# Performance work log

Measured on AMD Instinct MI355X. Metric: run time of the kernel, lower is better.

The kernel has to match this reference:

```python
import jax, jax.numpy as jnp
import numpy as np

B, N, E, H = 8, 512, 1024, 128   # graphs, nodes, edges, hidden
T = 8                             # num_edge_types
HOPS = 3                          # graph_hops


def setup_inputs() -> dict:
    key = jax.random.key(0)
    ks = jax.random.split(key, 10)
    node_feature = jax.random.normal(ks[0], (B, N, H), dtype=jnp.float32)
    edge_vec = jax.random.randint(ks[1], (B, E), 0, T)  # per-edge type ids
    # sparse incidence matrices (one-hot edge endpoints), as the scipy .A densification does
    src = jax.random.randint(ks[2], (B, E), 0, N)
    tgt = jax.random.randint(ks[3], (B, E), 0, N)
    node2edge = jax.nn.one_hot(src, N, dtype=jnp.float32)                 # [B,E,N]
    edge2node = jnp.swapaxes(jax.nn.one_hot(tgt, N, dtype=jnp.float32), 1, 2)  # [B,N,E]
    s = 0.02  # xavier-ish init scale
    edge_weight_tensor = jax.random.normal(ks[4], (T, H * H), dtype=jnp.float32) * s
    Wz = jax.random.normal(ks[5], (2 * H, H), dtype=jnp.float32) * s
    Wr = jax.random.normal(ks[6], (2 * H, H), dtype=jnp.float32) * s
    Wt = jax.random.normal(ks[7], (2 * H, H), dtype=jnp.float32) * s
    Wf = jax.random.normal(ks[8], (4 * H, H), dtype=jnp.float32) * s
    bf = jnp.zeros((H,), dtype=jnp.float32)
    return {"node_feature": node_feature, "edge_vec": edge_vec,
            "node2edge": node2edge, "edge2node": edge2node,
            "edge_weight_tensor": edge_weight_tensor,
            "Wz": Wz, "Wr": Wr, "Wt": Wt, "Wf": Wf, "bf": bf}


def reference(node_feature, edge_vec, node2edge, edge2node,
              edge_weight_tensor, Wz, Wr, Wt, Wf, bf):
    Hd = node_feature.shape[-1]
    # gather per-edge weight matrices once (edge_vec is constant across hops)
    Wedge = edge_weight_tensor[edge_vec].reshape(edge_vec.shape + (Hd, Hd))  # [B,E,H,H]

    def mp(h, n2e, e2n):
        emb = jnp.einsum('ben,bnh->beh', n2e, h)          # gather node states to edges
        new = jnp.einsum('behd,bed->beh', Wedge, emb)     # per-edge-type matvec
        return jnp.einsum('bne,beh->bnh', e2n, new)       # scatter-aggregate to nodes

    def gru_step(h, a):
        x = jnp.concatenate([h, a], axis=-1)
        z = jax.nn.sigmoid(x @ Wz)
        r = jax.nn.sigmoid(x @ Wr)
        t = jnp.tanh(jnp.concatenate([r * h, a], axis=-1) @ Wt)
        return (1.0 - z) * h + z * t

    h = node_feature
    for _ in range(HOPS):
        bw = mp(h, node2edge, edge2node)
        fw = mp(h, jnp.swapaxes(edge2node, 1, 2), jnp.swapaxes(node2edge, 1, 2))
        # GatedFusion(fw, bw)
        z = jax.nn.sigmoid(jnp.concatenate([fw, bw, fw * bw, fw - bw], axis=-1) @ Wf + bf)
        agg = (1.0 - z) * fw + z * bw
        h = gru_step(h, agg)
    return h
```

## Files before the change

kernel.cpp:

```cpp
#include <hip/hip_runtime.h>

#define Bb 8
#define Nn 512
#define Ee 1024
#define Hh 128
#define Tt 8
#define FPAD 132

__device__ __forceinline__ float sigm(float x){ return 1.0f/(1.0f + __expf(-x)); }
__device__ __forceinline__ float tanh_fast(float x){ return 2.0f/(1.0f + __expf(-2.0f*x)) - 1.0f; }

__device__ __forceinline__ void fma4(float* acc, float4 x, float4 w0, float4 w1, float4 w2, float4 w3){
  acc[0] += x.x*w0.x + x.y*w1.x + x.z*w2.x + x.w*w3.x;
  acc[1] += x.x*w0.y + x.y*w1.y + x.z*w2.y + x.w*w3.y;
  acc[2] += x.x*w0.z + x.y*w1.z + x.z*w2.z + x.w*w3.z;
  acc[3] += x.x*w0.w + x.y*w1.w + x.z*w2.w + x.w*w3.w;
}

__global__ void k_extract(const float4* __restrict__ n2e, const float4* __restrict__ e2n,
                          int* __restrict__ src, int* __restrict__ tgt){
  const int total1 = Bb*Ee*Nn/4;
  for (int i = blockIdx.x*blockDim.x + threadIdx.x; i < total1; i += gridDim.x*blockDim.x){
    float4 v = n2e[i];
    if (v.x!=0.f || v.y!=0.f || v.z!=0.f || v.w!=0.f){
      int base = i*4;
      int row = base >> 9;
      int n   = base & 511;
      if (v.x!=0.f) src[row] = n;
      if (v.y!=0.f) src[row] = n+1;
      if (v.z!=0.f) src[row] = n+2;
      if (v.w!=0.f) src[row] = n+3;
    }
  }
  const int total2 = Bb*Nn*Ee/4;
  for (int i = blockIdx.x*blockDim.x + threadIdx.x; i < total2; i += gridDim.x*blockDim.x){
    float4 v = e2n[i];
    if (v.x!=0.f || v.y!=0.f || v.z!=0.f || v.w!=0.f){
      int base = i*4;
      int row = base >> 10;
      int e   = base & 1023;
      int b = row >> 9, n = row & 511;
      int* tp = tgt + b*Ee;
      if (v.x!=0.f) tp[e]   = n;
      if (v.y!=0.f) tp[e+1] = n;
      if (v.z!=0.f) tp[e+2] = n;
      if (v.w!=0.f) tp[e+3] = n;
    }
  }
}

__global__ void k_transW(const float* __restrict__ W, float* __restrict__ WT){
  int i = blockIdx.x*blockDim.x + threadIdx.x;
  if (i >= Tt*Hh*Hh) return;
  int t = i >> 14;
  int h = (i >> 7) & 127;
  int d = i & 127;
  WT[(t*Hh + d)*Hh + h] = W[i];
}

__global__ void k_prep(const float* __restrict__ Wf, float* __restrict__ Ff){
  int i = blockIdx.x*blockDim.x + threadIdx.x;
  if (i >= 384*Hh) return;
  int r = i >> 7, c = i & 127;
  float v;
  if (r < 128)      v = Wf[r*Hh + c] + Wf[(r+384)*Hh + c];
  else if (r < 256) v = Wf[r*Hh + c] - Wf[(r+256)*Hh + c];
  else              v = Wf[r*Hh + c];
  Ff[i] = v;
}

__global__ void k_sort(const int* __restrict__ ev, int* __restrict__ order, int* __restrict__ offs){
  __shared__ int cnt[Tt], offs_s[Tt+1], pos[Tt];
  int b = blockIdx.x, tid = threadIdx.x;
  if (tid < Tt) cnt[tid] = 0;
  __syncthreads();
  for (int e = tid; e < Ee; e += blockDim.x) atomicAdd(&cnt[ev[b*Ee+e]], 1);
  __syncthreads();
  if (tid == 0){ offs_s[0]=0; for (int t=0;t<Tt;t++) offs_s[t+1]=offs_s[t]+cnt[t]; }
  __syncthreads();
  if (tid < Tt) pos[tid] = offs_s[tid];
  if (tid < Tt+1) offs[b*(Tt+1)+tid] = offs_s[tid];
  __syncthreads();
  for (int e = tid; e < Ee; e += blockDim.x){
    int t = ev[b*Ee+e];
    int p = atomicAdd(&pos[t], 1);
    order[b*Ee + p] = e;
  }
}

__global__ __launch_bounds__(256) void k_edge_mp(
    const float* __restrict__ h, const float* __restrict__ WT,
    const int* __restrict__ order, const int* __restrict__ offs,
    const int* __restrict__ src, const int* __restrict__ tgt,
    float* __restrict__ bw, float* __restrict__ fw)
{
  int x = blockIdx.x;
  int dir = x & 1, bt = x >> 1, t = bt & 7, b = bt >> 3;
  int beg = offs[b*(Tt+1)+t], end = offs[b*(Tt+1)+t+1];
  int chunk0 = beg + blockIdx.y*32;
  if (chunk0 >= end) return;
  const int* gI = dir ? tgt : src;
  const int* sI = dir ? src : tgt;
  float* out = dir ? fw : bw;

  __shared__ float sEmb[32][FPAD];
  __shared__ int sNode[32];
  int tid = threadIdx.x, lane = tid & 63, w = tid >> 6;
  int e0 = (lane >> 3)*4;
  int c0 = w*32 + (lane & 7)*4;
  const float* __restrict__ Wg = WT + t*Hh*Hh + c0;

  for (int chunk = chunk0; chunk < end; chunk += gridDim.y*32){
    int ne = min(32, end - chunk);
    __syncthreads();
    {
      int ir = tid >> 5, k0 = (tid & 31)*4;
      #pragma unroll
      for (int rr = 0; rr < 4; ++rr){
        int e = ir + rr*8;
        float4 v = {0.f,0.f,0.f,0.f};
        if (e < ne){
          int eid = order[b*Ee + chunk + e];
          v = *(const float4*)&h[(size_t)(b*Nn + gI[b*Ee + eid])*Hh + k0];
        }
        *(float4*)&sEmb[e][k0] = v;
      }
      if (tid < 32){
        int nd = -1;
        if (tid < ne){ int eid = order[b*Ee + chunk + tid]; nd = sI[b*Ee + eid]; }
        sNode[tid] = nd;
      }
    }
    __syncthreads();

    float acc[4][4] = {};
    #pragma unroll 4
    for (int k = 0; k < Hh; k += 4){
      float4 w0 = *(const float4*)&Wg[(size_t)(k+0)*Hh];
      float4 w1 = *(const float4*)&Wg[(size_t)(k+1)*Hh];
      float4 w2 = *(const float4*)&Wg[(size_t)(k+2)*Hh];
      float4 w3 = *(const float4*)&Wg[(size_t)(k+3)*Hh];
      #pragma unroll
      for (int j = 0; j < 4; ++j){
        float4 xv = *(const float4*)&sEmb[e0+j][k];
        fma4(acc[j], xv, w0, w1, w2, w3);
      }
    }
    #pragma unroll
    for (int j = 0; j < 4; ++j){
      int node = sNode[e0+j];
      if (node >= 0){
        float* op = out + (size_t)(b*Nn + node)*Hh + c0;
        atomicAdd(op+0, acc[j][0]);
        atomicAdd(op+1, acc[j][1]);
        atomicAdd(op+2, acc[j][2]);
        atomicAdd(op+3, acc[j][3]);
      }
    }
  }
}

__device__ __forceinline__ void gemm_sec(const float (*X)[FPAD], int r,
                                         const float* __restrict__ Wg, float* acc){
  #pragma unroll 4
  for (int k = 0; k < 128; k += 4){
    float4 x  = *(const float4*)&X[r][k];
    float4 w0 = *(const float4*)&Wg[(size_t)(k+0)*Hh];
    float4 w1 = *(const float4*)&Wg[(size_t)(k+1)*Hh];
    float4 w2 = *(const float4*)&Wg[(size_t)(k+2)*Hh];
    float4 w3 = *(const float4*)&Wg[(size_t)(k+3)*Hh];
    fma4(acc, x, w0, w1, w2, w3);
  }
}

__device__ __forceinline__ void gemm_prod(const float (*A)[FPAD], const float (*B)[FPAD], int r,
                                          const float* __restrict__ Wg, float* acc){
  #pragma unroll 4
  for (int k = 0; k < 128; k += 4){
    float4 a = *(const float4*)&A[r][k];
    float4 b = *(const float4*)&B[r][k];
    float4 x = make_float4(a.x*b.x, a.y*b.y, a.z*b.z, a.w*b.w);
    float4 w0 = *(const float4*)&Wg[(size_t)(k+0)*Hh];
    float4 w1 = *(const float4*)&Wg[(size_t)(k+1)*Hh];
    float4 w2 = *(const float4*)&Wg[(size_t)(k+2)*Hh];
    float4 w3 = *(const float4*)&Wg[(size_t)(k+3)*Hh];
    fma4(acc, x, w0, w1, w2, w3);
  }
}

__device__ __forceinline__ void gemm2(const float (*X)[FPAD], int r,
                                      const float* __restrict__ Wa, const float* __restrict__ Wb,
                                      float* acc1, float* acc2){
  #pragma unroll 4
  for (int k = 0; k < 128; k += 4){
    float4 x  = *(const float4*)&X[r][k];
    float4 a0 = *(const float4*)&Wa[(size_t)(k+0)*Hh];
    float4 a1 = *(const float4*)&Wa[(size_t)(k+1)*Hh];
    float4 a2 = *(const float4*)&Wa[(size_t)(k+2)*Hh];
    float4 a3 = *(const float4*)&Wa[(size_t)(k+3)*Hh];
    fma4(acc1, x, a0, a1, a2, a3);
    float4 b0 = *(const float4*)&Wb[(size_t)(k+0)*Hh];
    float4 b1 = *(const float4*)&Wb[(size_t)(k+1)*Hh];
    float4 b2 = *(const float4*)&Wb[(size_t)(k+2)*Hh];
    float4 b3 = *(const float4*)&Wb[(size_t)(k+3)*Hh];
    fma4(acc2, x, b0, b1, b2, b3);
  }
}

__global__ __launch_bounds__(512) void k_fuse_gru(
    const float* __restrict__ hin, const float* __restrict__ fw, const float* __restrict__ bw,
    const float* __restrict__ Ff, const float* __restrict__ bfv,
    const float* __restrict__ Wz, const float* __restrict__ Wr, const float* __restrict__ Wt,
    float* __restrict__ hout, float* __restrict__ zf, float* __restrict__ zb)
{
  __shared__ float sF[16][FPAD];
  __shared__ float sS[16][FPAD];
  __shared__ float sH[16][FPAD];
  int tid  = threadIdx.x;
  int row0 = blockIdx.x * 16;
  int lane = tid & 63, w = tid >> 6;
  int r    = lane >> 2;
  int c0   = w*16 + (lane & 3)*4;

  {
    int ir = tid >> 5, k0 = (tid & 31)*4;
    size_t g = (size_t)(row0 + ir)*Hh + k0;
    *(float4*)&sF[ir][k0] = *(const float4*)&fw[g];
    *(float4*)&sS[ir][k0] = *(const float4*)&bw[g];
    *(float4*)&sH[ir][k0] = *(const float4*)&hin[g];
  }
  float4 bias = *(const float4*)&bfv[c0];
  __syncthreads();

  float af[4] = {0,0,0,0};
  gemm_sec (sF, r, Ff + c0,            af);
  gemm_sec (sS, r, Ff + 128*Hh + c0,   af);
  gemm_prod(sF, sS, r, Ff + 256*Hh + c0, af);

  float agv[4];
  {
    float bb[4] = {bias.x, bias.y, bias.z, bias.w};
    #pragma unroll
    for (int j = 0; j < 4; ++j){
      float z = sigm(af[j] + bb[j]);
      agv[j] = (1.0f - z)*sF[r][c0+j] + z*sS[r][c0+j];
    }
  }
  __syncthreads();
  *(float4*)&sF[r][c0] = make_float4(agv[0], agv[1], agv[2], agv[3]);
  __syncthreads();

  float az[4] = {0,0,0,0}, ar[4] = {0,0,0,0};
  gemm2(sH, r, Wz + c0,          Wr + c0,          az, ar);
  gemm2(sF, r, Wz + 128*Hh + c0, Wr + 128*Hh + c0, az, ar);

  float zz[4];
  {
    float rh[4];
    #pragma unroll
    for (int j = 0; j < 4; ++j){
      zz[j] = sigm(az[j]);
      rh[j] = sigm(ar[j]) * sH[r][c0+j];
    }
    *(float4*)&sS[r][c0] = make_float4(rh[0], rh[1], rh[2], rh[3]);
  }
  __syncthreads();

  float at[4] = {0,0,0,0};
  gemm_sec(sS, r, Wt + c0,          at);
  gemm_sec(sF, r, Wt + 128*Hh + c0, at);

  float o[4];
  #pragma unroll
  for (int j = 0; j < 4; ++j){
    float t = tanh_fast(at[j]);
    o[j] = (1.0f - zz[j])*sH[r][c0+j] + zz[j]*t;
  }
  *(float4*)&hout[(size_t)(row0 + r)*Hh + c0] = make_float4(o[0], o[1], o[2], o[3]);

  {
    int ir = tid >> 5, k0 = (tid & 31)*4;
    size_t g = (size_t)(row0 + ir)*Hh + k0;
    float4 zv = {0.f,0.f,0.f,0.f};
    *(float4*)&zf[g] = zv;
    *(float4*)&zb[g] = zv;
  }
}

extern "C" void kernel_launch(void* const* d_in, const int* in_sizes, int n_in,
                              void* d_out, int out_size, void* d_ws, size_t ws_size,
                              hipStream_t stream){
  const float* node_feature = (const float*)d_in[0];
  const int*   edge_vec     = (const int*)d_in[1];
  const float* n2e          = (const float*)d_in[2];
  const float* e2n          = (const float*)d_in[3];
  const float* Wtensor      = (const float*)d_in[4];
  const float* Wz           = (const float*)d_in[5];
  const float* Wr           = (const float*)d_in[6];
  const float* Wt           = (const float*)d_in[7];
  const float* Wf           = (const float*)d_in[8];
  const float* bf           = (const float*)d_in[9];
  float* out = (float*)d_out;

  char* p = (char*)d_ws;
  int* src   = (int*)p; p += Bb*Ee*4;
  int* tgt   = (int*)p; p += Bb*Ee*4;
  int* order = (int*)p; p += Bb*Ee*4;
  int* offs  = (int*)p; p += 4096;
  float* WT  = (float*)p; p += (size_t)Tt*Hh*Hh*4;
  float* Ff  = (float*)p; p += (size_t)384*Hh*4;
  float* bwp = (float*)p; p += (size_t)Bb*Nn*Hh*4;
  float* fwp = (float*)p; p += (size_t)Bb*Nn*Hh*4;
  float* h1  = (float*)p; p += (size_t)Bb*Nn*Hh*4;

  k_extract<<<1024, 256, 0, stream>>>((const float4*)n2e, (const float4*)e2n, src, tgt);
  k_transW<<<(Tt*Hh*Hh + 255)/256, 256, 0, stream>>>(Wtensor, WT);
  k_prep<<<(384*Hh + 255)/256, 256, 0, stream>>>(Wf, Ff);
  k_sort<<<Bb, 256, 0, stream>>>(edge_vec, order, offs);
  hipMemsetAsync(bwp, 0, (size_t)2*Bb*Nn*Hh*4, stream);

  const float* hin = node_feature;
  float* houts[3] = { out, h1, out };
  for (int hop = 0; hop < 3; ++hop){
    k_edge_mp<<<dim3(Bb*Tt*2, 4), 256, 0, stream>>>(hin, WT, order, offs, src, tgt, bwp, fwp);
    k_fuse_gru<<<(Bb*Nn)/16, 512, 0, stream>>>(hin, fwp, bwp, Ff, bf, Wz, Wr, Wt, houts[hop], fwp, bwp);
    hin = houts[hop];
  }
}
```

Measured before the change: 474.4 us.

## Double-buffer register prefetch in GEMM loops and retile fuse-GRU blocks

The inner k-loops of the edge message-passing matvec and the fusion/GRU GEMM helpers become fully unrolled loops that double-buffer weight and activation loads in registers, so the next step's global and LDS reads are issued before the current step's FMAs. k_fuse_gru moves from 16 rows with 512 threads to 8 rows with 256 threads, giving each thread a wider column span and launching twice as many blocks. Both kernels gain a launch-bounds occupancy hint of 2, and the edge kernel's LDS row padding changes to 136. Holding two large register buffers raises register pressure, which could force spills or lower occupancy.

```diff
diff --git a/kernel.cpp b/kernel.cpp
--- a/kernel.cpp
+++ b/kernel.cpp
@@ -6,6 +6,7 @@
 #define Hh 128
 #define Tt 8
 #define FPAD 132
+#define EPAD 136
 
 __device__ __forceinline__ float sigm(float x){ return 1.0f/(1.0f + __expf(-x)); }
 __device__ __forceinline__ float tanh_fast(float x){ return 2.0f/(1.0f + __expf(-2.0f*x)) - 1.0f; }
@@ -88,7 +89,7 @@
   }
 }
 
-__global__ __launch_bounds__(256) void k_edge_mp(
+__global__ __launch_bounds__(256, 2) void k_edge_mp(
     const float* __restrict__ h, const float* __restrict__ WT,
     const int* __restrict__ order, const int* __restrict__ offs,
     const int* __restrict__ src, const int* __restrict__ tgt,
@@ -103,7 +104,7 @@
   const int* sI = dir ? src : tgt;
   float* out = dir ? fw : bw;
 
-  __shared__ float sEmb[32][FPAD];
+  __shared__ float sEmb[32][EPAD];
   __shared__ int sNode[32];
   int tid = threadIdx.x, lane = tid & 63, w = tid >> 6;
   int e0 = (lane >> 3)*4;
@@ -134,18 +135,33 @@
     __syncthreads();
 
     float acc[4][4] = {};
-    #pragma unroll 4
-    for (int k = 0; k < Hh; k += 4){
-      float4 w0 = *(const float4*)&Wg[(size_t)(k+0)*Hh];
-      float4 w1 = *(const float4*)&Wg[(size_t)(k+1)*Hh];
-      float4 w2 = *(const float4*)&Wg[(size_t)(k+2)*Hh];
-      float4 w3 = *(const float4*)&Wg[(size_t)(k+3)*Hh];
-      #pragma unroll
-      for (int j = 0; j < 4; ++j){
-        float4 xv = *(const float4*)&sEmb[e0+j][k];
-        fma4(acc[j], xv, w0, w1, w2, w3);
-      }
-    }
+    float4 wb[2][8], xe[2][4][2];
+    #pragma unroll
+    for (int j = 0; j < 8; ++j) wb[0][j] = *(const float4*)&Wg[j*Hh];
+    #pragma unroll
+    for (int je = 0; je < 4; ++je){
+      xe[0][je][0] = *(const float4*)&sEmb[e0+je][0];
+      xe[0][je][1] = *(const float4*)&sEmb[e0+je][4];
+    }
+    #pragma unroll
+    for (int s = 0; s < 16; ++s){
+      const int cur = s & 1, nxt = cur ^ 1;
+      if (s < 15){
+        #pragma unroll
+        for (int j = 0; j < 8; ++j) wb[nxt][j] = *(const float4*)&Wg[((s+1)*8 + j)*Hh];
+        #pragma unroll
+        for (int je = 0; je < 4; ++je){
+          xe[nxt][je][0] = *(const float4*)&sEmb[e0+je][(s+1)*8];
+          xe[nxt][je][1] = *(const float4*)&sEmb[e0+je][(s+1)*8 + 4];
+        }
+      }
+      #pragma unroll
+      for (int je = 0; je < 4; ++je){
+        fma4(acc[je], xe[cur][je][0], wb[cur][0], wb[cur][1], wb[cur][2], wb[cur][3]);
+        fma4(acc[je], xe[cur][je][1], wb[cur][4], wb[cur][5], wb[cur][6], wb[cur][7]);
+      }
+    }
+
     #pragma unroll
     for (int j = 0; j < 4; ++j){
       int node = sNode[e0+j];
@@ -160,67 +176,98 @@
   }
 }
 
+
 __device__ __forceinline__ void gemm_sec(const float (*X)[FPAD], int r,
                                          const float* __restrict__ Wg, float* acc){
-  #pragma unroll 4
-  for (int k = 0; k < 128; k += 4){
-    float4 x  = *(const float4*)&X[r][k];
-    float4 w0 = *(const float4*)&Wg[(size_t)(k+0)*Hh];
-    float4 w1 = *(const float4*)&Wg[(size_t)(k+1)*Hh];
-    float4 w2 = *(const float4*)&Wg[(size_t)(k+2)*Hh];
-    float4 w3 = *(const float4*)&Wg[(size_t)(k+3)*Hh];
-    fma4(acc, x, w0, w1, w2, w3);
+  float4 wb[2][16], xb[2][4];
+  #pragma unroll
+  for (int j = 0; j < 16; ++j) wb[0][j] = *(const float4*)&Wg[j*Hh];
+  #pragma unroll
+  for (int q = 0; q < 4; ++q) xb[0][q] = *(const float4*)&X[r][q*4];
+  #pragma unroll
+  for (int s = 0; s < 8; ++s){
+    const int cur = s & 1, nxt = cur ^ 1;
+    if (s < 7){
+      #pragma unroll
+      for (int j = 0; j < 16; ++j) wb[nxt][j] = *(const float4*)&Wg[((s+1)*16 + j)*Hh];
+      #pragma unroll
+      for (int q = 0; q < 4; ++q) xb[nxt][q] = *(const float4*)&X[r][(s+1)*16 + q*4];
+    }
+    #pragma unroll
+    for (int q = 0; q < 4; ++q)
+      fma4(acc, xb[cur][q], wb[cur][4*q+0], wb[cur][4*q+1], wb[cur][4*q+2], wb[cur][4*q+3]);
   }
 }
 
 __device__ __forceinline__ void gemm_prod(const float (*A)[FPAD], const float (*B)[FPAD], int r,
                                           const float* __restrict__ Wg, float* acc){
-  #pragma unroll 4
-  for (int k = 0; k < 128; k += 4){
-    float4 a = *(const float4*)&A[r][k];
-    float4 b = *(const float4*)&B[r][k];
-    float4 x = make_float4(a.x*b.x, a.y*b.y, a.z*b.z, a.w*b.w);
-    float4 w0 = *(const float4*)&Wg[(size_t)(k+0)*Hh];
-    float4 w1 = *(const float4*)&Wg[(size_t)(k+1)*Hh];
-    float4 w2 = *(const float4*)&Wg[(size_t)(k+2)*Hh];
-    float4 w3 = *(const float4*)&Wg[(size_t)(k+3)*Hh];
-    fma4(acc, x, w0, w1, w2, w3);
+  float4 wb[2][16], xa[2][4], xc[2][4];
+  #pragma unroll
+  for (int j = 0; j < 16; ++j) wb[0][j] = *(const float4*)&Wg[j*Hh];
+  #pragma unroll
+  for (int q = 0; q < 4; ++q){ xa[0][q] = *(const float4*)&A[r][q*4]; xc[0][q] = *(const float4*)&B[r][q*4]; }
+  #pragma unroll
+  for (int s = 0; s < 8; ++s){
+    const int cur = s & 1, nxt = cur ^ 1;
+    if (s < 7){
+      #pragma unroll
+      for (int j = 0; j < 16; ++j) wb[nxt][j] = *(const float4*)&Wg[((s+1)*16 + j)*Hh];
+      #pragma unroll
+      for (int q = 0; q < 4; ++q){
+        xa[nxt][q] = *(const float4*)&A[r][(s+1)*16 + q*4];
+        xc[nxt][q] = *(const float4*)&B[r][(s+1)*16 + q*4];
+      }
+    }
+    #pragma unroll
+    for (int q = 0; q < 4; ++q){
+      float4 a = xa[cur][q], c = xc[cur][q];
+      float4 xv = make_float4(a.x*c.x, a.y*c.y, a.z*c.z, a.w*c.w);
+      fma4(acc, xv, wb[cur][4*q+0], wb[cur][4*q+1], wb[cur][4*q+2], wb[cur][4*q+3]);
+    }
   }
 }
 
 __device__ __forceinline__ void gemm2(const float (*X)[FPAD], int r,
-                                      const float* __restrict__ Wa, const float* __restrict__ Wb,
+                                      const float* __restrict__ Wa, const float* __restrict__ Wc,
                                       float* acc1, float* acc2){
-  #pragma unroll 4
-  for (int k = 0; k < 128; k += 4){
-    float4 x  = *(const float4*)&X[r][k];
-    float4 a0 = *(const float4*)&Wa[(size_t)(k+0)*Hh];
-    float4 a1 = *(const float4*)&Wa[(size_t)(k+1)*Hh];
-    float4 a2 = *(const float4*)&Wa[(size_t)(k+2)*Hh];
-    float4 a3 = *(const float4*)&Wa[(size_t)(k+3)*Hh];
-    fma4(acc1, x, a0, a1, a2, a3);
-    float4 b0 = *(const float4*)&Wb[(size_t)(k+0)*Hh];
-    float4 b1 = *(const float4*)&Wb[(size_t)(k+1)*Hh];
-    float4 b2 = *(const float4*)&Wb[(size_t)(k+2)*Hh];
-    float4 b3 = *(const float4*)&Wb[(size_t)(k+3)*Hh];
-    fma4(acc2, x, b0, b1, b2, b3);
-  }
-}
-
-__global__ __launch_bounds__(512) void k_fuse_gru(
+  float4 wa[2][8], wc[2][8], xb[2][2];
+  #pragma unroll
+  for (int j = 0; j < 8; ++j){ wa[0][j] = *(const float4*)&Wa[j*Hh]; wc[0][j] = *(const float4*)&Wc[j*Hh]; }
+  xb[0][0] = *(const float4*)&X[r][0];
+  xb[0][1] = *(const float4*)&X[r][4];
+  #pragma unroll
+  for (int s = 0; s < 16; ++s){
+    const int cur = s & 1, nxt = cur ^ 1;
+    if (s < 15){
+      #pragma unroll
+      for (int j = 0; j < 8; ++j){
+        wa[nxt][j] = *(const float4*)&Wa[((s+1)*8 + j)*Hh];
+        wc[nxt][j] = *(const float4*)&Wc[((s+1)*8 + j)*Hh];
+      }
+      xb[nxt][0] = *(const float4*)&X[r][(s+1)*8];
+      xb[nxt][1] = *(const float4*)&X[r][(s+1)*8 + 4];
+    }
+    fma4(acc1, xb[cur][0], wa[cur][0], wa[cur][1], wa[cur][2], wa[cur][3]);
+    fma4(acc1, xb[cur][1], wa[cur][4], wa[cur][5], wa[cur][6], wa[cur][7]);
+    fma4(acc2, xb[cur][0], wc[cur][0], wc[cur][1], wc[cur][2], wc[cur][3]);
+    fma4(acc2, xb[cur][1], wc[cur][4], wc[cur][5], wc[cur][6], wc[cur][7]);
+  }
+}
+
+__global__ __launch_bounds__(256, 2) void k_fuse_gru(
     const float* __restrict__ hin, const float* __restrict__ fw, const float* __restrict__ bw,
     const float* __restrict__ Ff, const float* __restrict__ bfv,
     const float* __restrict__ Wz, const float* __restrict__ Wr, const float* __restrict__ Wt,
     float* __restrict__ hout, float* __restrict__ zf, float* __restrict__ zb)
 {
-  __shared__ float sF[16][FPAD];
-  __shared__ float sS[16][FPAD];
-  __shared__ float sH[16][FPAD];
+  __shared__ float sF[8][FPAD];
+  __shared__ float sS[8][FPAD];
+  __shared__ float sH[8][FPAD];
   int tid  = threadIdx.x;
-  int row0 = blockIdx.x * 16;
+  int row0 = blockIdx.x * 8;
   int lane = tid & 63, w = tid >> 6;
-  int r    = lane >> 2;
-  int c0   = w*16 + (lane & 3)*4;
+  int r    = lane >> 3;
+  int c0   = w*32 + (lane & 7)*4;
 
   {
     int ir = tid >> 5, k0 = (tid & 31)*4;
@@ -233,8 +280,8 @@
   __syncthreads();
 
   float af[4] = {0,0,0,0};
-  gemm_sec (sF, r, Ff + c0,            af);
-  gemm_sec (sS, r, Ff + 128*Hh + c0,   af);
+  gemm_sec (sF, r, Ff + c0,              af);
+  gemm_sec (sS, r, Ff + 128*Hh + c0,     af);
   gemm_prod(sF, sS, r, Ff + 256*Hh + c0, af);
 
   float agv[4];
@@ -323,7 +370,7 @@
   float* houts[3] = { out, h1, out };
   for (int hop = 0; hop < 3; ++hop){
     k_edge_mp<<<dim3(Bb*Tt*2, 4), 256, 0, stream>>>(hin, WT, order, offs, src, tgt, bwp, fwp);
-    k_fuse_gru<<<(Bb*Nn)/16, 512, 0, stream>>>(hin, fwp, bwp, Ff, bf, Wz, Wr, Wt, houts[hop], fwp, bwp);
+    k_fuse_gru<<<(Bb*Nn)/8, 256, 0, stream>>>(hin, fwp, bwp, Ff, bf, Wz, Wr, Wt, houts[hop], fwp, bwp);
     hin = houts[hop];
   }
 }
```

Result: slower. 1.551 ms (+227.1%).

## Drop shared staging and register double-buffer loads in edge and GRU kernels

Applied to the files above, without the earlier changes.

The edge message-passing kernel no longer stages gathered node rows into shared memory. It reads them straight from global memory with a two-stage register prefetch of both the weights and the activations. The fused gate/GRU kernel is resized to 8 rows and 256 threads. It reads fw, bw and h rows directly from global memory with double-buffered register loads, and keeps only the intermediate rows in shared memory, which removes staging barriers. The aim is to hide load latency and cut synchronisation, at the cost of more redundant global and cache traffic and higher register pressure.

```diff
diff --git a/kernel.cpp b/kernel.cpp
--- a/kernel.cpp
+++ b/kernel.cpp
@@ -86,6 +86,15 @@
     int p = atomicAdd(&pos[t], 1);
     order[b*Ee + p] = e;
   }
+}
+
+__device__ __forceinline__ void ldw4(float4* b, const float* __restrict__ W, int k0){
+  #pragma unroll
+  for (int j = 0; j < 4; ++j) b[j] = *(const float4*)&W[(k0+j)*Hh];
+}
+__device__ __forceinline__ void ldw8(float4* b, const float* __restrict__ W, int k0){
+  #pragma unroll
+  for (int j = 0; j < 8; ++j) b[j] = *(const float4*)&W[(k0+j)*Hh];
 }
 
 __global__ __launch_bounds__(256) void k_edge_mp(
@@ -103,8 +112,8 @@
   const int* sI = dir ? src : tgt;
   float* out = dir ? fw : bw;
 
-  __shared__ float sEmb[32][FPAD];
-  __shared__ int sNode[32];
+  __shared__ int sGat[32];
+  __shared__ int sSc[32];
   int tid = threadIdx.x, lane = tid & 63, w = tid >> 6;
   int e0 = (lane >> 3)*4;
   int c0 = w*32 + (lane & 7)*4;
@@ -113,42 +122,50 @@
   for (int chunk = chunk0; chunk < end; chunk += gridDim.y*32){
     int ne = min(32, end - chunk);
     __syncthreads();
-    {
-      int ir = tid >> 5, k0 = (tid & 31)*4;
+    if (tid < 32){
+      int ng = -1, ns = -1;
+      if (tid < ne){
+        int eid = order[b*Ee + chunk + tid];
+        ng = gI[b*Ee + eid];
+        ns = sI[b*Ee + eid];
+      }
+      sGat[tid] = ng; sSc[tid] = ns;
+    }
+    __syncthreads();
+
+    const float* xr[4];
+    int nsc[4];
+    #pragma unroll
+    for (int je = 0; je < 4; ++je){
+      int ng = sGat[e0+je];
+      xr[je] = h + (size_t)(b*Nn + (ng < 0 ? 0 : ng))*Hh;
+      nsc[je] = sSc[e0+je];
+    }
+
+    float acc[4][4] = {};
+    float4 wA[4], wB[4], xA[4], xB[4];
+    ldw4(wA, Wg, 0);
+    #pragma unroll
+    for (int je = 0; je < 4; ++je) xA[je] = *(const float4*)&xr[je][0];
+    #pragma unroll
+    for (int s = 0; s < 32; s += 2){
+      ldw4(wB, Wg, (s+1)*4);
       #pragma unroll
-      for (int rr = 0; rr < 4; ++rr){
-        int e = ir + rr*8;
-        float4 v = {0.f,0.f,0.f,0.f};
-        if (e < ne){
-          int eid = order[b*Ee + chunk + e];
-          v = *(const float4*)&h[(size_t)(b*Nn + gI[b*Ee + eid])*Hh + k0];
-        }
-        *(float4*)&sEmb[e][k0] = v;
+      for (int je = 0; je < 4; ++je) xB[je] = *(const float4*)&xr[je][(s+1)*4];
+      #pragma unroll
+      for (int je = 0; je < 4; ++je) fma4(acc[je], xA[je], wA[0], wA[1], wA[2], wA[3]);
+      if (s+2 < 32){
+        ldw4(wA, Wg, (s+2)*4);
+        #pragma unroll
+        for (int je = 0; je < 4; ++je) xA[je] = *(const float4*)&xr[je][(s+2)*4];
       }
-      if (tid < 32){
-        int nd = -1;
-        if (tid < ne){ int eid = order[b*Ee + chunk + tid]; nd = sI[b*Ee + eid]; }
-        sNode[tid] = nd;
-      }
-    }
-    __syncthreads();
-
-    float acc[4][4] = {};
-    #pragma unroll 4
-    for (int k = 0; k < Hh; k += 4){
-      float4 w0 = *(const float4*)&Wg[(size_t)(k+0)*Hh];
-      float4 w1 = *(const float4*)&Wg[(size_t)(k+1)*Hh];
-      float4 w2 = *(const float4*)&Wg[(size_t)(k+2)*Hh];
-      float4 w3 = *(const float4*)&Wg[(size_t)(k+3)*Hh];
       #pragma unroll
-      for (int j = 0; j < 4; ++j){
-        float4 xv = *(const float4*)&sEmb[e0+j][k];
-        fma4(acc[j], xv, w0, w1, w2, w3);
-      }
-    }
+      for (int je = 0; je < 4; ++je) fma4(acc[je], xB[je], wB[0], wB[1], wB[2], wB[3]);
+    }
+
     #pragma unroll
     for (int j = 0; j < 4; ++j){
-      int node = sNode[e0+j];
+      int node = nsc[j];
       if (node >= 0){
         float* op = out + (size_t)(b*Nn + node)*Hh + c0;
         atomicAdd(op+0, acc[j][0]);
@@ -160,121 +177,149 @@
   }
 }
 
-__device__ __forceinline__ void gemm_sec(const float (*X)[FPAD], int r,
+
+__device__ __forceinline__ void sec_row(const float* __restrict__ xrow,
+                                        const float* __restrict__ Wg, float* acc){
+  float4 wA[8], wB[8], xA0, xA1, xB0, xB1;
+  ldw8(wA, Wg, 0);
+  xA0 = *(const float4*)&xrow[0]; xA1 = *(const float4*)&xrow[4];
+  #pragma unroll
+  for (int s = 0; s < 16; s += 2){
+    ldw8(wB, Wg, (s+1)*8);
+    xB0 = *(const float4*)&xrow[(s+1)*8]; xB1 = *(const float4*)&xrow[(s+1)*8+4];
+    fma4(acc, xA0, wA[0], wA[1], wA[2], wA[3]);
+    fma4(acc, xA1, wA[4], wA[5], wA[6], wA[7]);
+    if (s+2 < 16){
+      ldw8(wA, Wg, (s+2)*8);
+      xA0 = *(const float4*)&xrow[(s+2)*8]; xA1 = *(const float4*)&xrow[(s+2)*8+4];
+    }
+    fma4(acc, xB0, wB[0], wB[1], wB[2], wB[3]);
+    fma4(acc, xB1, wB[4], wB[5], wB[6], wB[7]);
+  }
+}
+
+__device__ __forceinline__ void sec_prod(const float* __restrict__ ar_, const float* __restrict__ br_,
                                          const float* __restrict__ Wg, float* acc){
-  #pragma unroll 4
-  for (int k = 0; k < 128; k += 4){
-    float4 x  = *(const float4*)&X[r][k];
-    float4 w0 = *(const float4*)&Wg[(size_t)(k+0)*Hh];
-    float4 w1 = *(const float4*)&Wg[(size_t)(k+1)*Hh];
-    float4 w2 = *(const float4*)&Wg[(size_t)(k+2)*Hh];
-    float4 w3 = *(const float4*)&Wg[(size_t)(k+3)*Hh];
-    fma4(acc, x, w0, w1, w2, w3);
-  }
-}
-
-__device__ __forceinline__ void gemm_prod(const float (*A)[FPAD], const float (*B)[FPAD], int r,
-                                          const float* __restrict__ Wg, float* acc){
-  #pragma unroll 4
-  for (int k = 0; k < 128; k += 4){
-    float4 a = *(const float4*)&A[r][k];
-    float4 b = *(const float4*)&B[r][k];
-    float4 x = make_float4(a.x*b.x, a.y*b.y, a.z*b.z, a.w*b.w);
-    float4 w0 = *(const float4*)&Wg[(size_t)(k+0)*Hh];
-    float4 w1 = *(const float4*)&Wg[(size_t)(k+1)*Hh];
-    float4 w2 = *(const float4*)&Wg[(size_t)(k+2)*Hh];
-    float4 w3 = *(const float4*)&Wg[(size_t)(k+3)*Hh];
-    fma4(acc, x, w0, w1, w2, w3);
-  }
-}
-
-__device__ __forceinline__ void gemm2(const float (*X)[FPAD], int r,
-                                      const float* __restrict__ Wa, const float* __restrict__ Wb,
-                                      float* acc1, float* acc2){
-  #pragma unroll 4
-  for (int k = 0; k < 128; k += 4){
-    float4 x  = *(const float4*)&X[r][k];
-    float4 a0 = *(const float4*)&Wa[(size_t)(k+0)*Hh];
-    float4 a1 = *(const float4*)&Wa[(size_t)(k+1)*Hh];
-    float4 a2 = *(const float4*)&Wa[(size_t)(k+2)*Hh];
-    float4 a3 = *(const float4*)&Wa[(size_t)(k+3)*Hh];
-    fma4(acc1, x, a0, a1, a2, a3);
-    float4 b0 = *(const float4*)&Wb[(size_t)(k+0)*Hh];
-    float4 b1 = *(const float4*)&Wb[(size_t)(k+1)*Hh];
-    float4 b2 = *(const float4*)&Wb[(size_t)(k+2)*Hh];
-    float4 b3 = *(const float4*)&Wb[(size_t)(k+3)*Hh];
-    fma4(acc2, x, b0, b1, b2, b3);
-  }
-}
-
-__global__ __launch_bounds__(512) void k_fuse_gru(
+  float4 wA[8], wB[8];
+  float4 xA0, xA1, xB0, xB1;
+  ldw8(wA, Wg, 0);
+  {
+    float4 a0 = *(const float4*)&ar_[0], b0 = *(const float4*)&br_[0];
+    float4 a1 = *(const float4*)&ar_[4], b1 = *(const float4*)&br_[4];
+    xA0 = make_float4(a0.x*b0.x, a0.y*b0.y, a0.z*b0.z, a0.w*b0.w);
+    xA1 = make_float4(a1.x*b1.x, a1.y*b1.y, a1.z*b1.z, a1.w*b1.w);
+  }
+  #pragma unroll
+  for (int s = 0; s < 16; s += 2){
+    ldw8(wB, Wg, (s+1)*8);
+    {
+      float4 a0 = *(const float4*)&ar_[(s+1)*8],   b0 = *(const float4*)&br_[(s+1)*8];
+      float4 a1 = *(const float4*)&ar_[(s+1)*8+4], b1 = *(const float4*)&br_[(s+1)*8+4];
+      xB0 = make_float4(a0.x*b0.x, a0.y*b0.y, a0.z*b0.z, a0.w*b0.w);
+      xB1 = make_float4(a1.x*b1.x, a1.y*b1.y, a1.z*b1.z, a1.w*b1.w);
+    }
+    fma4(acc, xA0, wA[0], wA[1], wA[2], wA[3]);
+    fma4(acc, xA1, wA[4], wA[5], wA[6], wA[7]);
+    if (s+2 < 16){
+      ldw8(wA, Wg, (s+2)*8);
+      float4 a0 = *(const float4*)&ar_[(s+2)*8],   b0 = *(const float4*)&br_[(s+2)*8];
+      float4 a1 = *(const float4*)&ar_[(s+2)*8+4], b1 = *(const float4*)&br_[(s+2)*8+4];
+      xA0 = make_float4(a0.x*b0.x, a0.y*b0.y, a0.z*b0.z, a0.w*b0.w);
+      xA1 = make_float4(a1.x*b1.x, a1.y*b1.y, a1.z*b1.z, a1.w*b1.w);
+    }
+    fma4(acc, xB0, wB[0], wB[1], wB[2], wB[3]);
+    fma4(acc, xB1, wB[4], wB[5], wB[6], wB[7]);
+  }
+}
+
+__device__ __forceinline__ void sec2(const float* __restrict__ xrow,
+                                     const float* __restrict__ Wa, const float* __restrict__ Wc,
+                                     float* acc1, float* acc2){
+  float4 aA[4], aB[4], cA[4], cB[4], xA, xB;
+  ldw4(aA, Wa, 0); ldw4(cA, Wc, 0);
+  xA = *(const float4*)&xrow[0];
+  #pragma unroll
+  for (int s = 0; s < 32; s += 2){
+    ldw4(aB, Wa, (s+1)*4); ldw4(cB, Wc, (s+1)*4);
+    xB = *(const float4*)&xrow[(s+1)*4];
+    fma4(acc1, xA, aA[0], aA[1], aA[2], aA[3]);
+    fma4(acc2, xA, cA[0], cA[1], cA[2], cA[3]);
+    if (s+2 < 32){
+      ldw4(aA, Wa, (s+2)*4); ldw4(cA, Wc, (s+2)*4);
+      xA = *(const float4*)&xrow[(s+2)*4];
+    }
+    fma4(acc1, xB, aB[0], aB[1], aB[2], aB[3]);
+    fma4(acc2, xB, cB[0], cB[1], cB[2], cB[3]);
+  }
+}
+
+__global__ __launch_bounds__(256) void k_fuse_gru(
     const float* __restrict__ hin, const float* __restrict__ fw, const float* __restrict__ bw,
     const float* __restrict__ Ff, const float* __restrict__ bfv,
     const float* __restrict__ Wz, const float* __restrict__ Wr, const float* __restrict__ Wt,
     float* __restrict__ hout, float* __restrict__ zf, float* __restrict__ zb)
 {
-  __shared__ float sF[16][FPAD];
-  __shared__ float sS[16][FPAD];
-  __shared__ float sH[16][FPAD];
+  __shared__ float sA[8][FPAD];
+  __shared__ float sR[8][FPAD];
   int tid  = threadIdx.x;
-  int row0 = blockIdx.x * 16;
+  int row0 = blockIdx.x * 8;
   int lane = tid & 63, w = tid >> 6;
-  int r    = lane >> 2;
-  int c0   = w*16 + (lane & 3)*4;
+  int r    = lane >> 3;
+  int c0   = w*32 + (lane & 7)*4;
+
+  const float* __restrict__ frow = fw  + (size_t)(row0 + r)*Hh;
+  const float* __restrict__ brow = bw  + (size_t)(row0 + r)*Hh;
+  const float* __restrict__ hrow = hin + (size_t)(row0 + r)*Hh;
+  float4 bias = *(const float4*)&bfv[c0];
+
+  float af[4] = {0,0,0,0};
+  sec_row (frow, Ff + c0,            af);
+  sec_row (brow, Ff + 128*Hh + c0,   af);
+  sec_prod(frow, brow, Ff + 256*Hh + c0, af);
 
   {
-    int ir = tid >> 5, k0 = (tid & 31)*4;
-    size_t g = (size_t)(row0 + ir)*Hh + k0;
-    *(float4*)&sF[ir][k0] = *(const float4*)&fw[g];
-    *(float4*)&sS[ir][k0] = *(const float4*)&bw[g];
-    *(float4*)&sH[ir][k0] = *(const float4*)&hin[g];
-  }
-  float4 bias = *(const float4*)&bfv[c0];
-  __syncthreads();
-
-  float af[4] = {0,0,0,0};
-  gemm_sec (sF, r, Ff + c0,            af);
-  gemm_sec (sS, r, Ff + 128*Hh + c0,   af);
-  gemm_prod(sF, sS, r, Ff + 256*Hh + c0, af);
-
-  float agv[4];
-  {
+    float4 fv = *(const float4*)&frow[c0];
+    float4 bv = *(const float4*)&brow[c0];
     float bb[4] = {bias.x, bias.y, bias.z, bias.w};
+    float fvv[4] = {fv.x, fv.y, fv.z, fv.w};
+    float bvv[4] = {bv.x, bv.y, bv.z, bv.w};
+    float ag[4];
     #pragma unroll
     for (int j = 0; j < 4; ++j){
       float z = sigm(af[j] + bb[j]);
-      agv[j] = (1.0f - z)*sF[r][c0+j] + z*sS[r][c0+j];
-    }
-  }
-  __syncthreads();
-  *(float4*)&sF[r][c0] = make_float4(agv[0], agv[1], agv[2], agv[3]);
-  __syncthreads();
+      ag[j] = (1.0f - z)*fvv[j] + z*bvv[j];
+    }
+    *(float4*)&sA[r][c0] = make_float4(ag[0], ag[1], ag[2], ag[3]);
+  }
 
   float az[4] = {0,0,0,0}, ar[4] = {0,0,0,0};
-  gemm2(sH, r, Wz + c0,          Wr + c0,          az, ar);
-  gemm2(sF, r, Wz + 128*Hh + c0, Wr + 128*Hh + c0, az, ar);
-
-  float zz[4];
+  sec2(hrow, Wz + c0, Wr + c0, az, ar);
+  __syncthreads();
+  sec2(&sA[r][0], Wz + 128*Hh + c0, Wr + 128*Hh + c0, az, ar);
+
+  float zz[4], hv[4];
   {
+    float4 hv4 = *(const float4*)&hrow[c0];
+    hv[0]=hv4.x; hv[1]=hv4.y; hv[2]=hv4.z; hv[3]=hv4.w;
     float rh[4];
     #pragma unroll
     for (int j = 0; j < 4; ++j){
       zz[j] = sigm(az[j]);
-      rh[j] = sigm(ar[j]) * sH[r][c0+j];
-    }
-    *(float4*)&sS[r][c0] = make_float4(rh[0], rh[1], rh[2], rh[3]);
-  }
-  __syncthreads();
+      rh[j] = sigm(ar[j]) * hv[j];
+    }
+    *(float4*)&sR[r][c0] = make_float4(rh[0], rh[1], rh[2], rh[3]);
+  }
 
   float at[4] = {0,0,0,0};
-  gemm_sec(sS, r, Wt + c0,          at);
-  gemm_sec(sF, r, Wt + 128*Hh + c0, at);
+  sec_row(&sA[r][0], Wt + 128*Hh + c0, at);
+  __syncthreads();
+  sec_row(&sR[r][0], Wt + c0, at);
 
   float o[4];
   #pragma unroll
   for (int j = 0; j < 4; ++j){
     float t = tanh_fast(at[j]);
-    o[j] = (1.0f - zz[j])*sH[r][c0+j] + zz[j]*t;
+    o[j] = (1.0f - zz[j])*hv[j] + zz[j]*t;
   }
   *(float4*)&hout[(size_t)(row0 + r)*Hh + c0] = make_float4(o[0], o[1], o[2], o[3]);
 
@@ -323,7 +368,7 @@
   float* houts[3] = { out, h1, out };
   for (int hop = 0; hop < 3; ++hop){
     k_edge_mp<<<dim3(Bb*Tt*2, 4), 256, 0, stream>>>(hin, WT, order, offs, src, tgt, bwp, fwp);
-    k_fuse_gru<<<(Bb*Nn)/16, 512, 0, stream>>>(hin, fwp, bwp, Ff, bf, Wz, Wr, Wt, houts[hop], fwp, bwp);
+    k_fuse_gru<<<(Bb*Nn)/8, 256, 0, stream>>>(hin, fwp, bwp, Ff, bf, Wz, Wr, Wt, houts[hop], fwp, bwp);
     hin = houts[hop];
   }
 }
```

New measurement: 1.565 ms. 230% more time.
